# Optimization experiments

Hardware: AMD Instinct MI355X
Metric: run time of the kernel (lower is better)

The kernel has to match this reference:

```python
import jax, jax.numpy as jnp
import numpy as np

T, B = 32, 64
H, W = 16, 16
FEAT = 32
CNN_DIM = 512
N_ACT = 5
MAP_OUT = FEAT * H * W  # 8192, flattened map readout


def _conv_relu(x, w, b, stride):
    y = jax.lax.conv_general_dilated(
        x, w, (stride, stride), 'VALID',
        dimension_numbers=('NCHW', 'OIHW', 'NCHW'))
    return jax.nn.relu(y + b[None, :, None, None])


def _mlp(x, w1, b1, w2, b2):
    return jax.nn.relu(x @ w1 + b1) @ w2 + b2


def setup_inputs() -> dict:
    key = jax.random.key(0)
    ks = jax.random.split(key, 32)
    g = lambda k, shape, fan: jax.random.normal(k, shape, jnp.float32) * (1.0 / np.sqrt(fan))
    inp = {}
    inp['image'] = jax.random.uniform(ks[0], (T * B, 84, 84, 3), jnp.float32) * 255.0
    inp['done'] = jnp.zeros((T, B), jnp.float32)
    inp['state0'] = jnp.zeros((B, FEAT, H, W), jnp.float32)
    inp['position'] = jax.random.randint(ks[1], (T * B, 2), 0, H).astype(jnp.int32)
    # NatureCNN params
    inp['w1'] = g(ks[2], (32, 3, 8, 8), 3 * 8 * 8); inp['b1'] = jnp.zeros((32,), jnp.float32)
    inp['w2'] = g(ks[3], (64, 32, 4, 4), 32 * 4 * 4); inp['b2'] = jnp.zeros((64,), jnp.float32)
    inp['w3'] = g(ks[4], (64, 64, 3, 3), 64 * 3 * 3); inp['b3'] = jnp.zeros((64,), jnp.float32)
    inp['wfc'] = g(ks[5], (64 * 7 * 7, CNN_DIM), 64 * 7 * 7); inp['bfc'] = jnp.zeros((CNN_DIM,), jnp.float32)
    # Map write projection
    inp['Ww'] = g(ks[6], (CNN_DIM, FEAT), CNN_DIM); inp['bw'] = jnp.zeros((FEAT,), jnp.float32)
    # pos_net MLP: one-hot(16)+one-hot(16)=32 -> 64
    inp['wp1'] = g(ks[7], (2 * H, 64), 2 * H); inp['bp1'] = jnp.zeros((64,), jnp.float32)
    inp['wp2'] = g(ks[8], (64, 64), 64); inp['bp2'] = jnp.zeros((64,), jnp.float32)
    # policy MLP: (MAP_OUT+64) -> 64 -> N_ACT
    inp['wpo1'] = g(ks[9], (MAP_OUT + 64, 64), MAP_OUT + 64); inp['bpo1'] = jnp.zeros((64,), jnp.float32)
    inp['wpo2'] = g(ks[10], (64, N_ACT), 64) * 0.01; inp['bpo2'] = jnp.zeros((N_ACT,), jnp.float32)
    # value MLP
    inp['wv1'] = g(ks[11], (MAP_OUT + 64, 64), MAP_OUT + 64); inp['bv1'] = jnp.zeros((64,), jnp.float32)
    inp['wv2'] = g(ks[12], (64, 1), 64); inp['bv2'] = jnp.zeros((1,), jnp.float32)
    return inp


def reference(image, done, state0, w1, b1, w2, b2, w3, b3, wfc, bfc, Ww, bw,
              wp1, bp1, wp2, bp2, wpo1, bpo1, wpo2, bpo2, wv1, bv1, wv2, bv2,
              position):
    # preprocess_image: /255 and NHWC -> NCHW
    x = jnp.transpose(image / 255.0, (0, 3, 1, 2))
    x = _conv_relu(x, w1, b1, 4)   # [TB,32,20,20]
    x = _conv_relu(x, w2, b2, 2)   # [TB,64,9,9]
    x = _conv_relu(x, w3, b3, 1)   # [TB,64,7,7]
    h = jax.nn.relu(x.reshape(x.shape[0], -1) @ wfc + bfc)  # [TB,512]

    h_seq = h.reshape(T, B, CNN_DIM)
    idx_seq = position.reshape(T, B, 2)
    benv = jnp.arange(B)

    def step(state, inp):
        h_t, d_t, i_t = inp
        masked = (1.0 - d_t)[:, None, None, None] * state  # reset done envs
        wfeat = h_t @ Ww + bw                              # [B,FEAT]
        state = masked.at[benv, :, i_t[:, 0], i_t[:, 1]].add(wfeat)
        return state, state.reshape(B, -1)                 # per-step map readout

    state, outs = jax.lax.scan(step, state0, (h_seq, done, idx_seq))
    hidden = outs.reshape(T * B, MAP_OUT)

    # position net on one-hot coords
    pos_oh = jnp.concatenate([jax.nn.one_hot(position[:, 0], H, dtype=hidden.dtype),
                              jax.nn.one_hot(position[:, 1], W, dtype=hidden.dtype)], axis=1)
    pos_feat = _mlp(pos_oh, wp1, bp1, wp2, bp2)            # [TB,64]
    hidden = jnp.concatenate([hidden, pos_feat], axis=1)

    logits = _mlp(hidden, wpo1, bpo1, wpo2, bpo2)          # [TB,N_ACT]
    v = _mlp(hidden, wv1, bv1, wv2, bv2)                   # [TB,1]
    return logits, v, state
```

## Files before the change

kernel.cpp:

```cpp
#include <hip/hip_runtime.h>
#include <hip/hip_bf16.h>


#define TT 32
#define BB 64
#define TBR 2048

typedef _Float16 half_t;
typedef __attribute__((ext_vector_type(4))) _Float16 half4;
typedef __attribute__((ext_vector_type(8))) _Float16 half8;
typedef __attribute__((ext_vector_type(4))) float f32x4;

#define OFF_W1T   0u
#define OFF_W2T   6144u
#define OFF_W3T   22528u
#define OFF_WF    40960u
#define OFF_PF    106496u
#define OFF_Y0    237568u
#define OFF_PP    245760u
#define OFF_H     507904u
#define OFF_DELTA 1556480u
#define OFF_WFCT  1818624u
#define OFF_C3    2621440u
#define OFF_H1    5832704u

__global__ __launch_bounds__(256) void prep_all(
    const float* __restrict__ w1, const float* __restrict__ w2,
    const float* __restrict__ w3, half_t* __restrict__ w1p,
    half_t* __restrict__ w2T, half_t* __restrict__ w3T,
    const float* __restrict__ wfc, half_t* __restrict__ wfcT) {
  __shared__ float t[32][33];
  int bx = blockIdx.x;
  if (bx < 304) {
    int g = bx * 256 + threadIdx.x;
    if (g < 8192) {
      int kk = g & 31, oc = (g >> 5) & 31, tap = g >> 10;
      half_t v = (half_t)0.f;
      if (kk < 24) {
        int kx = kk / 3, c = kk - 3 * kx;
        v = (half_t)(w1[oc * 192 + c * 64 + tap * 8 + kx] * (1.0f / 255.0f));
      }
      w1p[g] = v;
      return;
    }
    int g2 = g - 8192;
    if (g2 < 32768) {
      int c = g2 & 31, oc = (g2 >> 5) & 63, tap = g2 >> 11;
      w2T[g2] = (half_t)w2[oc * 512 + c * 16 + tap];
      return;
    }
    int g3 = g2 - 32768;
    if (g3 < 36864) {
      int c = g3 & 63, oc = (g3 >> 6) & 63, tap = g3 >> 12;
      w3T[g3] = (half_t)w3[oc * 576 + c * 9 + tap];
    }
    return;
  }
  int gb = bx - 304;
  int k0 = (gb % 98) * 32, n0 = (gb / 98) * 32;
  int tx = threadIdx.x & 31, ty = threadIdx.x >> 5;
#pragma unroll
  for (int i = 0; i < 4; ++i)
    t[ty + 8 * i][tx] = wfc[(size_t)(k0 + ty + 8 * i) * 512 + n0 + tx];
  __syncthreads();
#pragma unroll
  for (int i = 0; i < 4; ++i)
    wfcT[(size_t)(n0 + ty + 8 * i) * 3136 + k0 + tx] =
        (half_t)t[tx][ty + 8 * i];
}

#define C1_BANDF 5040
#define C1_BANDV 1260
#define C1OUT_OFF 20672
#define C1A(ip, bp)                                                     \
  (C1OUT_OFF + ((ip) >> 1) * 128 +                                      \
   (((((ip) & 1) << 6) | ((bp) & 0x30)) ^ ((((ip) >> 1) & 7) << 4)) +   \
   ((bp) & 15))
#define C2A(ir, bp) \
  ((ir) * 128 + (((bp) & 0x70) ^ (((ir) & 7) << 4)) + ((bp) & 15))
__global__ __launch_bounds__(256) void conv123_mfma(
    const float* __restrict__ img, const half_t* __restrict__ w1p,
    const float* __restrict__ b1, const half_t* __restrict__ w2T,
    const float* __restrict__ b2, const half_t* __restrict__ w3T,
    const float* __restrict__ b3, half_t* __restrict__ out) {
  __shared__ __align__(16) char lds[46272];
  half_t (*stag)[C1_BANDF] = (half_t(*)[C1_BANDF])lds;
  int tid = threadIdx.x;
  int li = blockIdx.x;
  int w = tid >> 6, l = tid & 63, lc = l & 15, q = l >> 4;
  const float* ib = img + (size_t)li * 21168;

  half8 bfrag1[8][2];
#pragma unroll
  for (int tap = 0; tap < 8; ++tap)
#pragma unroll
    for (int t = 0; t < 2; ++t)
      bfrag1[tap][t] =
          *(const half8*)(w1p + (size_t)(tap * 32 + t * 16 + lc) * 32 + q * 8);
  float b1v[2] = {b1[lc], b1[16 + lc]};

  f32x4 fr[5];
#define C1_LOADB(b)                                                   \
  {                                                                   \
    const float* src = ib + 4032 * (b);                               \
    _Pragma("unroll") for (int i = 0; i < 5; ++i) {                   \
      int g = tid + 256 * i;                                          \
      if (g < C1_BANDV) fr[i] = *(const f32x4*)(src + 4 * g);         \
    }                                                                 \
  }
#define C1_WRITEB(buf)                                                \
  {                                                                   \
    _Pragma("unroll") for (int i = 0; i < 5; ++i) {                   \
      int g = tid + 256 * i;                                          \
      if (g < C1_BANDV) {                                             \
        half4 o;                                                      \
        _Pragma("unroll") for (int j = 0; j < 4; ++j)                 \
            o[j] = (half_t)fr[i][j];                                  \
        *(half4*)&stag[buf][4 * g] = o;                               \
      }                                                               \
    }                                                                 \
  }

  C1_LOADB(0);
  C1_WRITEB(0);
  for (int b = 0; b < 5; ++b) {
    if (b < 4) C1_LOADB(b + 1);
    __syncthreads();
    int buf = b & 1;
    for (int tile = w; tile < 5; tile += 4) {
      int lp = tile * 16 + lc;
      int oyl = lp / 20, ox = lp - oyl * 20;
      f32x4 acc[2];
      acc[0] = (f32x4){0.f, 0.f, 0.f, 0.f};
      acc[1] = (f32x4){0.f, 0.f, 0.f, 0.f};
#pragma unroll
      for (int ky = 0; ky < 8; ++ky) {
        half8 af;
        if (q < 3) {
          const half_t* p = &stag[buf][(4 * oyl + ky) * 252 + 12 * ox + q * 8];
          *(half4*)&af = *(const half4*)p;
          *((half4*)&af + 1) = *((const half4*)(p + 4));
        } else {
#pragma unroll
          for (int j = 0; j < 8; ++j) af[j] = (half_t)0.f;
        }
        acc[0] = __builtin_amdgcn_mfma_f32_16x16x32_f16(af, bfrag1[ky][0],
                                                        acc[0], 0, 0, 0);
        acc[1] = __builtin_amdgcn_mfma_f32_16x16x32_f16(af, bfrag1[ky][1],
                                                        acc[1], 0, 0, 0);
      }
#pragma unroll
      for (int t = 0; t < 2; ++t) {
#pragma unroll
        for (int r = 0; r < 4; ++r) {
          int ip = b * 80 + tile * 16 + q * 4 + r;
          int ch = t * 16 + lc;
          *(half_t*)(lds + C1A(ip, 2 * ch)) =
              (half_t)fmaxf(acc[t][r] + b1v[t], 0.f);
        }
      }
    }
    if (b < 4) C1_WRITEB((b + 1) & 1);
  }
  __syncthreads();

  {
    half8 bfrag2[16][2];
#pragma unroll
    for (int tap = 0; tap < 16; ++tap)
#pragma unroll
      for (int j = 0; j < 2; ++j) {
        int nt = (w & 1) * 2 + j;
        bfrag2[tap][j] = *(const half8*)(
            w2T + (size_t)(tap * 64 + nt * 16 + lc) * 32 + q * 8);
      }
    float b2v[2];
#pragma unroll
    for (int j = 0; j < 2; ++j) b2v[j] = b2[(w & 1) * 32 + j * 16 + lc];

#pragma unroll
    for (int ti = 0; ti < 3; ++ti) {
      int tile = (w >> 1) + 2 * ti;
      int row16 = tile * 16 + lc;
      int orow = row16 < 81 ? row16 : 80;
      int oy = orow / 9, ox = orow - oy * 9;
      f32x4 acc[2];
      acc[0] = (f32x4){0.f, 0.f, 0.f, 0.f};
      acc[1] = (f32x4){0.f, 0.f, 0.f, 0.f};
#pragma unroll
      for (int tap = 0; tap < 16; ++tap) {
        int ky = tap >> 2, kx = tap & 3;
        int ip = (2 * oy + ky) * 20 + 2 * ox + kx;
        half8 af = *(const half8*)(lds + C1A(ip, q * 16));
        acc[0] = __builtin_amdgcn_mfma_f32_16x16x32_f16(af, bfrag2[tap][0],
                                                        acc[0], 0, 0, 0);
        acc[1] = __builtin_amdgcn_mfma_f32_16x16x32_f16(af, bfrag2[tap][1],
                                                        acc[1], 0, 0, 0);
      }
#pragma unroll
      for (int j = 0; j < 2; ++j) {
#pragma unroll
        for (int r = 0; r < 4; ++r) {
          int mr = tile * 16 + q * 4 + r;
          if (mr < 81) {
            int col = (w & 1) * 32 + j * 16 + lc;
            *(half_t*)(lds + C2A(mr, 2 * col)) =
                (half_t)fmaxf(acc[j][r] + b2v[j], 0.f);
          }
        }
      }
    }
  }
  __syncthreads();

  {
    half8 bfrag3[9][2];
#pragma unroll
    for (int tap = 0; tap < 9; ++tap)
#pragma unroll
      for (int ch = 0; ch < 2; ++ch)
        bfrag3[tap][ch] = *(const half8*)(
            w3T + (size_t)(tap * 64 + w * 16 + lc) * 64 + ch * 32 + q * 8);
    float b3v = b3[w * 16 + lc];

    half_t* ob = out + (size_t)li * 3136;
#pragma unroll
    for (int tile = 0; tile < 4; ++tile) {
      int row16 = tile * 16 + lc;
      int orow = row16 < 49 ? row16 : 48;
      int oy = orow / 7, ox = orow - oy * 7;
      f32x4 acc = (f32x4){0.f, 0.f, 0.f, 0.f};
#pragma unroll
      for (int tap = 0; tap < 9; ++tap) {
        int ky = tap / 3, kx = tap - ky * 3;
        int ir = (oy + ky) * 9 + ox + kx;
#pragma unroll
        for (int ch = 0; ch < 2; ++ch) {
          half8 af = *(const half8*)(lds + C2A(ir, ch * 64 + q * 16));
          acc = __builtin_amdgcn_mfma_f32_16x16x32_f16(af, bfrag3[tap][ch],
                                                       acc, 0, 0, 0);
        }
      }
#pragma unroll
      for (int r = 0; r < 4; ++r) {
        int pos = tile * 16 + q * 4 + r;
        if (pos < 49) {
          int col = w * 16 + lc;
          ob[(size_t)col * 49 + pos] = (half_t)fmaxf(acc[r] + b3v, 0.f);
        }
      }
    }
  }
}

__global__ __launch_bounds__(256) void fc_mfma(
    const half_t* __restrict__ A, const half_t* __restrict__ Bt,
    float* __restrict__ h0, float* __restrict__ h1) {
  __shared__ __align__(16) half_t As[2][64 * 40];
  __shared__ __align__(16) half_t Bs[2][64 * 40];
  int tid = threadIdx.x;
  int m0 = blockIdx.y * 64, n0 = blockIdx.x * 64;
  int kh = blockIdx.z;
  int w = tid >> 6;
  int l = tid & 63;
  int lc = l & 15, q = l >> 4;
  int srow = tid >> 2, sseg = tid & 3;

  const half_t* aPtr = A + (size_t)(m0 + srow) * 3136 + kh * 1568 + sseg * 8;
  const half_t* bPtr = Bt + (size_t)(n0 + srow) * 3136 + kh * 1568 + sseg * 8;
  uint4 aReg = *(const uint4*)aPtr;
  uint4 bReg = *(const uint4*)bPtr;

  f32x4 acc[4];
#pragma unroll
  for (int t = 0; t < 4; ++t) acc[t] = (f32x4){0.f, 0.f, 0.f, 0.f};

  for (int s = 0; s < 49; ++s) {
    int cur = s & 1;
    *(uint4*)&As[cur][srow * 40 + sseg * 8] = aReg;
    *(uint4*)&Bs[cur][srow * 40 + sseg * 8] = bReg;
    __syncthreads();
    if (s < 48) {
      aReg = *(const uint4*)(aPtr + (s + 1) * 32);
      bReg = *(const uint4*)(bPtr + (s + 1) * 32);
    }
    half8 af = *(const half8*)&As[cur][(w * 16 + lc) * 40 + q * 8];
#pragma unroll
    for (int t = 0; t < 4; ++t) {
      half8 bf = *(const half8*)&Bs[cur][(t * 16 + lc) * 40 + q * 8];
      acc[t] = __builtin_amdgcn_mfma_f32_16x16x32_f16(af, bf, acc[t], 0, 0, 0);
    }
  }
  float* H = kh ? h1 : h0;
#pragma unroll
  for (int t = 0; t < 4; ++t) {
#pragma unroll
    for (int r = 0; r < 4; ++r) {
      int row = m0 + w * 16 + q * 4 + r;
      int col = n0 + t * 16 + lc;
      H[(size_t)row * 512 + col] = acc[t][r];
    }
  }
}

__global__ __launch_bounds__(256) void mid1_kernel(
    const float* __restrict__ h0, const float* __restrict__ h1,
    const float* __restrict__ bfc, const float* __restrict__ Ww,
    const float* __restrict__ bw, float* __restrict__ wf,
    const int* __restrict__ pos, const float* __restrict__ wp1,
    const float* __restrict__ bp1, const float* __restrict__ wp2,
    const float* __restrict__ bp2, float* __restrict__ pf,
    const float* __restrict__ s0, const float* __restrict__ wpo1,
    const float* __restrict__ wv1, float* __restrict__ y0) {
  __shared__ float red[128];
  int bx = blockIdx.x;
  if (bx < 256) {
    int g = bx * 256 + threadIdx.x;
    int row = g >> 5, oc = g & 31;
    float acc = bw[oc];
    const float* hr0 = h0 + (size_t)row * 512;
    const float* hr1 = h1 + (size_t)row * 512;
#pragma unroll 8
    for (int k = 0; k < 512; ++k)
      acc += fmaxf(hr0[k] + hr1[k] + bfc[k], 0.f) * Ww[k * 32 + oc];
    wf[g] = acc;
    return;
  }
  if (bx < 768) {
    int row = ((bx - 256) * 256 + threadIdx.x) >> 6;
    int l = threadIdx.x & 63;
    int p0 = pos[row * 2], p1 = pos[row * 2 + 1];
    float t1 = fmaxf(wp1[p0 * 64 + l] + wp1[(16 + p1) * 64 + l] + bp1[l], 0.f);
    float acc = bp2[l];
#pragma unroll
    for (int k = 0; k < 64; ++k) acc += __shfl(t1, k) * wp2[k * 64 + l];
    pf[row * 64 + l] = acc;
    return;
  }
  int g = bx - 768;
  int b = g >> 5, kc = g & 31;
  int n = threadIdx.x & 127, kh = threadIdx.x >> 7;
  const float* W = (n < 64) ? (wpo1 + n) : (wv1 + (n - 64));
  int k0 = kc * 256 + kh * 128;
  const float* s = s0 + (size_t)b * 8192 + k0;
  float acc = 0.f;
#pragma unroll 8
  for (int j = 0; j < 128; ++j) acc += s[j] * W[(size_t)(k0 + j) * 64];
  if (kh) red[n] = acc;
  __syncthreads();
  if (!kh) atomicAdd(y0 + b * 128 + n, acc + red[n]);
}

__global__ __launch_bounds__(256) void mid2_kernel(
    const int* __restrict__ pos, const float* __restrict__ wf,
    const float* __restrict__ wpo1, const float* __restrict__ wv1,
    float* __restrict__ delta, const float* __restrict__ s0,
    const float* __restrict__ done, float* __restrict__ out_state,
    const float* __restrict__ pf, float* __restrict__ pp) {
  int bx = blockIdx.x;
  if (bx < 1024) {
    int row = bx * 2 + (threadIdx.x >> 7);
    int n = threadIdx.x & 127;
    const float* W = (n < 64) ? (wpo1 + n) : (wv1 + (n - 64));
    int off = pos[row * 2] * 16 + pos[row * 2 + 1];
    const float* wfr = wf + row * 32;
    float d = 0.f;
#pragma unroll
    for (int c = 0; c < 32; ++c) d += wfr[c] * W[(size_t)(c * 256 + off) * 64];
    delta[(size_t)row * 128 + n] = d;
    return;
  }
  if (bx < 1088) {
    int b = bx - 1024, tid = threadIdx.x;
    float s[32];
#pragma unroll
    for (int c = 0; c < 32; ++c) s[c] = s0[(size_t)b * 8192 + c * 256 + tid];
    for (int t = 0; t < TT; ++t) {
      int row = t * BB + b;
      float mask = 1.f - done[row];
      int off = pos[row * 2] * 16 + pos[row * 2 + 1];
#pragma unroll
      for (int c = 0; c < 32; ++c) s[c] *= mask;
      if (tid == off) {
#pragma unroll
        for (int c = 0; c < 32; ++c) s[c] += wf[row * 32 + c];
      }
    }
#pragma unroll
    for (int c = 0; c < 32; ++c)
      out_state[(size_t)b * 8192 + c * 256 + tid] = s[c];
    return;
  }
  int row = (bx - 1088) * 2 + (threadIdx.x >> 7);
  int n = threadIdx.x & 127;
  const float* W = (n < 64) ? (wpo1 + n) : (wv1 + (n - 64));
  const float* pfr = pf + row * 64;
  float acc = 0.f;
#pragma unroll
  for (int k = 0; k < 64; ++k) acc += pfr[k] * W[(size_t)(8192 + k) * 64];
  pp[(size_t)row * 128 + n] = acc;
}

__global__ __launch_bounds__(128) void scan_head_kernel(
    const float* __restrict__ y0, const float* __restrict__ done,
    const float* __restrict__ delta, const float* __restrict__ pp,
    const float* __restrict__ bpo1, const float* __restrict__ bv1,
    const float* __restrict__ wpo2, const float* __restrict__ bpo2,
    const float* __restrict__ wv2, const float* __restrict__ bv2,
    float* __restrict__ logits, float* __restrict__ vout) {
  int b = blockIdx.x;
  int n = threadIdx.x;
  int l = n & 63, wv = n >> 6;
  float bias1 = wv ? bv1[l] : bpo1[l];
  float w2v[5];
  if (!wv) {
#pragma unroll
    for (int a = 0; a < 5; ++a) w2v[a] = wpo2[l * 5 + a];
  } else {
    w2v[0] = wv2[l];
  }
  float y = y0[b * 128 + n];
  for (int t = 0; t < TT; ++t) {
    int row = t * BB + b;
    y = y * (1.f - done[row]) + delta[(size_t)row * 128 + n];
    float act = fmaxf(y + pp[(size_t)row * 128 + n] + bias1, 0.f);
    if (!wv) {
#pragma unroll
      for (int a = 0; a < 5; ++a) {
        float pa = act * w2v[a];
#pragma unroll
        for (int m = 32; m >= 1; m >>= 1) pa += __shfl_xor(pa, m);
        if (l == 0) logits[row * 5 + a] = pa + bpo2[a];
      }
    } else {
      float pv = act * w2v[0];
#pragma unroll
      for (int m = 32; m >= 1; m >>= 1) pv += __shfl_xor(pv, m);
      if (l == 0) vout[row] = pv + bv2[0];
    }
  }
}

extern "C" void kernel_launch(void* const* d_in, const int* in_sizes, int n_in,
                              void* d_out, int out_size, void* d_ws, size_t ws_size,
                              hipStream_t stream) {
  const float* image = (const float*)d_in[0];
  const float* done = (const float*)d_in[1];
  const float* state0 = (const float*)d_in[2];
  const int* position = (const int*)d_in[3];
  const float* w1 = (const float*)d_in[4];
  const float* b1 = (const float*)d_in[5];
  const float* w2 = (const float*)d_in[6];
  const float* b2 = (const float*)d_in[7];
  const float* w3 = (const float*)d_in[8];
  const float* b3 = (const float*)d_in[9];
  const float* wfc = (const float*)d_in[10];
  const float* bfc = (const float*)d_in[11];
  const float* Ww = (const float*)d_in[12];
  const float* bw = (const float*)d_in[13];
  const float* wp1 = (const float*)d_in[14];
  const float* bp1 = (const float*)d_in[15];
  const float* wp2 = (const float*)d_in[16];
  const float* bp2 = (const float*)d_in[17];
  const float* wpo1 = (const float*)d_in[18];
  const float* bpo1 = (const float*)d_in[19];
  const float* wpo2 = (const float*)d_in[20];
  const float* bpo2 = (const float*)d_in[21];
  const float* wv1 = (const float*)d_in[22];
  const float* bv1 = (const float*)d_in[23];
  const float* wv2 = (const float*)d_in[24];
  const float* bv2 = (const float*)d_in[25];

  float* ws = (float*)d_ws;
  half_t* w1p = (half_t*)(ws + OFF_W1T);
  half_t* w2T = (half_t*)(ws + OFF_W2T);
  half_t* w3T = (half_t*)(ws + OFF_W3T);
  float* wf = ws + OFF_WF;
  float* pfb = ws + OFF_PF;
  float* y0 = ws + OFF_Y0;
  float* ppb = ws + OFF_PP;
  float* h0b = ws + OFF_H;
  float* h1b = ws + OFF_H1;
  float* deltab = ws + OFF_DELTA;
  half_t* wfcT = (half_t*)(ws + OFF_WFCT);
  half_t* c3b = (half_t*)(ws + OFF_C3);

  float* out = (float*)d_out;
  float* out_logits = out;
  float* out_v = out + 10240;
  float* out_state = out + 12288;

  hipMemsetAsync(y0, 0, 8192 * sizeof(float), stream);
  prep_all<<<1872, 256, 0, stream>>>(w1, w2, w3, w1p, w2T, w3T, wfc, wfcT);
  conv123_mfma<<<TBR, 256, 0, stream>>>(image, w1p, b1, w2T, b2, w3T, b3, c3b);
  fc_mfma<<<dim3(8, 32, 2), 256, 0, stream>>>(c3b, wfcT, h0b, h1b);
  mid1_kernel<<<2816, 256, 0, stream>>>(h0b, h1b, bfc, Ww, bw, wf, position,
                                        wp1, bp1, wp2, bp2, pfb, state0,
                                        wpo1, wv1, y0);
  mid2_kernel<<<2112, 256, 0, stream>>>(position, wf, wpo1, wv1, deltab,
                                        state0, done, out_state, pfb, ppb);
  scan_head_kernel<<<64, 128, 0, stream>>>(y0, done, deltab, ppb, bpo1, bv1,
                                           wpo2, bpo2, wv2, bv2,
                                           out_logits, out_v);
}
```

Baseline: 451.7 us.

## Stage conv1 image bands directly into LDS via async global_load_lds

The conv1 image bands are now copied straight from global memory into double-buffered LDS with global_load_lds, kept as fp32. Previously the data went through registers and was converted to fp16 before being written to LDS. Conversion to fp16 now happens when the MFMA operands are read, and the next band's load is issued before the current band is computed. The aim is to cut register staging and VALU work and to overlap the image fetch with compute. In exchange LDS use grows to about 64KB per block, which may lower occupancy, and LDS read traffic doubles.

Measured after the change: 454.2 us. Within noise of the previous version (+0.6%).

```diff
diff --git a/kernel.cpp b/kernel.cpp
--- a/kernel.cpp
+++ b/kernel.cpp
@@ -10,6 +10,8 @@
 typedef __attribute__((ext_vector_type(4))) _Float16 half4;
 typedef __attribute__((ext_vector_type(8))) _Float16 half8;
 typedef __attribute__((ext_vector_type(4))) float f32x4;
+typedef __attribute__((address_space(1))) const void gvoid1;
+typedef __attribute__((address_space(3))) void lvoid3;
 
 #define OFF_W1T   0u
 #define OFF_W2T   6144u
@@ -69,9 +71,8 @@
         (half_t)t[tx][ty + 8 * i];
 }
 
-#define C1_BANDF 5040
 #define C1_BANDV 1260
-#define C1OUT_OFF 20672
+#define C1OUT_OFF 40320
 #define C1A(ip, bp)                                                     \
   (C1OUT_OFF + ((ip) >> 1) * 128 +                                      \
    (((((ip) & 1) << 6) | ((bp) & 0x30)) ^ ((((ip) >> 1) & 7) << 4)) +   \
@@ -83,8 +84,7 @@
     const float* __restrict__ b1, const half_t* __restrict__ w2T,
     const float* __restrict__ b2, const half_t* __restrict__ w3T,
     const float* __restrict__ b3, half_t* __restrict__ out) {
-  __shared__ __align__(16) char lds[46272];
-  half_t (*stag)[C1_BANDF] = (half_t(*)[C1_BANDF])lds;
+  __shared__ __align__(16) char lds[65920];
   int tid = threadIdx.x;
   int li = blockIdx.x;
   int w = tid >> 6, l = tid & 63, lc = l & 15, q = l >> 4;
@@ -99,34 +99,24 @@
           *(const half8*)(w1p + (size_t)(tap * 32 + t * 16 + lc) * 32 + q * 8);
   float b1v[2] = {b1[lc], b1[16 + lc]};
 
-  f32x4 fr[5];
-#define C1_LOADB(b)                                                   \
+#define C1_STAGE(b, buf)                                              \
   {                                                                   \
     const float* src = ib + 4032 * (b);                               \
+    char* dbase = lds + (buf) * 20160;                                \
     _Pragma("unroll") for (int i = 0; i < 5; ++i) {                   \
       int g = tid + 256 * i;                                          \
-      if (g < C1_BANDV) fr[i] = *(const f32x4*)(src + 4 * g);         \
+      if (g < C1_BANDV)                                               \
+        __builtin_amdgcn_global_load_lds((gvoid1*)(src + 4 * g),      \
+                                         (lvoid3*)(dbase + 16 * g),   \
+                                         16, 0, 0);                   \
     }                                                                 \
   }
-#define C1_WRITEB(buf)                                                \
-  {                                                                   \
-    _Pragma("unroll") for (int i = 0; i < 5; ++i) {                   \
-      int g = tid + 256 * i;                                          \
-      if (g < C1_BANDV) {                                             \
-        half4 o;                                                      \
-        _Pragma("unroll") for (int j = 0; j < 4; ++j)                 \
-            o[j] = (half_t)fr[i][j];                                  \
-        *(half4*)&stag[buf][4 * g] = o;                               \
-      }                                                               \
-    }                                                                 \
-  }
-
-  C1_LOADB(0);
-  C1_WRITEB(0);
+
+  C1_STAGE(0, 0);
+  __syncthreads();
   for (int b = 0; b < 5; ++b) {
-    if (b < 4) C1_LOADB(b + 1);
-    __syncthreads();
-    int buf = b & 1;
+    if (b < 4) C1_STAGE(b + 1, (b + 1) & 1);
+    const float* bandp = (const float*)(lds + (b & 1) * 20160);
     for (int tile = w; tile < 5; tile += 4) {
       int lp = tile * 16 + lc;
       int oyl = lp / 20, ox = lp - oyl * 20;
@@ -137,9 +127,14 @@
       for (int ky = 0; ky < 8; ++ky) {
         half8 af;
         if (q < 3) {
-          const half_t* p = &stag[buf][(4 * oyl + ky) * 252 + 12 * ox + q * 8];
-          *(half4*)&af = *(const half4*)p;
-          *((half4*)&af + 1) = *((const half4*)(p + 4));
+          const float* p = bandp + (4 * oyl + ky) * 252 + 12 * ox + q * 8;
+          f32x4 v0 = *(const f32x4*)p;
+          f32x4 v1 = *(const f32x4*)(p + 4);
+#pragma unroll
+          for (int j = 0; j < 4; ++j) {
+            af[j] = (half_t)v0[j];
+            af[4 + j] = (half_t)v1[j];
+          }
         } else {
 #pragma unroll
           for (int j = 0; j < 8; ++j) af[j] = (half_t)0.f;
@@ -160,9 +155,8 @@
         }
       }
     }
-    if (b < 4) C1_WRITEB((b + 1) & 1);
-  }
-  __syncthreads();
+    __syncthreads();
+  }
 
   {
     half8 bfrag2[16][2];
@@ -243,10 +237,10 @@
       }
 #pragma unroll
       for (int r = 0; r < 4; ++r) {
-        int pos = tile * 16 + q * 4 + r;
-        if (pos < 49) {
+        int pos2 = tile * 16 + q * 4 + r;
+        if (pos2 < 49) {
           int col = w * 16 + lc;
-          ob[(size_t)col * 49 + pos] = (half_t)fmaxf(acc[r] + b3v, 0.f);
+          ob[(size_t)col * 49 + pos2] = (half_t)fmaxf(acc[r] + b3v, 0.f);
         }
       }
     }
```
